# Optimization experiments

Measured on AMD Instinct MI355X. Metric: run time of the kernel, lower is better.

## Reference

```python
import jax, jax.numpy as jnp
import numpy as np


def _pairwise_sqdist(a, b):
    # a: [B,N,3], b: [B,M,3] -> [B,N,M] squared L2 distances
    a2 = jnp.sum(a * a, axis=-1)            # [B,N]
    b2 = jnp.sum(b * b, axis=-1)            # [B,M]
    ab = jnp.einsum('bnd,bmd->bnm', a, b)   # [B,N,M]
    d = a2[:, :, None] + b2[:, None, :] - 2.0 * ab
    return jnp.maximum(d, 0.0)


def setup_inputs() -> dict:
    key = jax.random.key(0)
    k1, k2 = jax.random.split(key)
    B, N, M = 4, 8192, 8192
    p1 = jax.random.normal(k1, (B, N, 3), dtype=jnp.float32)
    p2 = jax.random.normal(k2, (B, M, 3), dtype=jnp.float32)
    return {"p1": p1, "p2": p2}


def reference(p1, p2):
    # chamfer_3DDist: squared L2 NN distances both directions, then mean of each
    d = _pairwise_sqdist(p1, p2)   # [B,N,M]
    d1 = jnp.min(d, axis=2)        # [B,N] nearest p2 for each p1 point
    d2 = jnp.min(d, axis=1)        # [B,M] nearest p1 for each p2 point
    return jnp.mean(d1) + jnp.mean(d2)
```

## Files before the change

kernel.cpp:

```cpp
#include <hip/hip_runtime.h>
#include <float.h>


#define BLK 256
#define CHUNK 2048
#define QPT 2
#define QPB (BLK * QPT)
#define B 4
#define NPTS 8192
#define TOTQ (2 * B * NPTS)

__global__ __launch_bounds__(BLK) void init_kernel(unsigned* mins, float* out, int n) {
    int i = blockIdx.x * BLK + threadIdx.x;
    if (i < n) mins[i] = 0x7F7FFFFFu;
    if (i == 0) out[0] = 0.f;
}

__global__ __launch_bounds__(BLK) void zero_out_kernel(float* out) {
    if (threadIdx.x == 0 && blockIdx.x == 0) out[0] = 0.f;
}

__global__ __launch_bounds__(BLK, 2) void cd_chunk_kernel(
    const float* __restrict__ p1, const float* __restrict__ p2,
    unsigned* __restrict__ mins)
{
    __shared__ float4 pts[CHUNK];
    int bid    = blockIdx.x;
    int mchunk = bid & 3;
    int qt     = (bid >> 2) & 15;
    int batch  = (bid >> 6) & 3;
    int dir    = bid >> 8;

    const float* qbase = (dir == 0 ? p1 : p2) + (size_t)batch * NPTS * 3;
    const float* dbase = (dir == 0 ? p2 : p1) + (size_t)batch * NPTS * 3;

    int tid = threadIdx.x;
    int mstart = mchunk * CHUNK;
    for (int j = tid; j < CHUNK; j += BLK) {
        const float* s = dbase + (size_t)(mstart + j) * 3;
        float x = s[0], y = s[1], z = s[2];
        pts[j] = make_float4(x, y, z, -0.5f * (x * x + y * y + z * z));
    }

    int q0 = qt * QPB + tid;
    int q1 = q0 + BLK;
    float ax = qbase[q0 * 3 + 0], ay = qbase[q0 * 3 + 1], az = qbase[q0 * 3 + 2];
    float bx = qbase[q1 * 3 + 0], by = qbase[q1 * 3 + 1], bz = qbase[q1 * 3 + 2];
    float an = ax * ax + ay * ay + az * az;
    float bn = bx * bx + by * by + bz * bz;
    __syncthreads();

    float sa0 = -FLT_MAX, sa1 = -FLT_MAX;
    float sb0 = -FLT_MAX, sb1 = -FLT_MAX;
    #pragma unroll 4
    for (int j = 0; j < CHUNK; j += 2) {
        float4 u = pts[j];
        float4 v = pts[j + 1];
        float s;
        s = fmaf(ax, u.x, u.w); s = fmaf(ay, u.y, s); s = fmaf(az, u.z, s); sa0 = fmaxf(sa0, s);
        s = fmaf(bx, u.x, u.w); s = fmaf(by, u.y, s); s = fmaf(bz, u.z, s); sb0 = fmaxf(sb0, s);
        s = fmaf(ax, v.x, v.w); s = fmaf(ay, v.y, s); s = fmaf(az, v.z, s); sa1 = fmaxf(sa1, s);
        s = fmaf(bx, v.x, v.w); s = fmaf(by, v.y, s); s = fmaf(bz, v.z, s); sb1 = fmaxf(sb1, s);
    }
    float da = fmaxf(an - 2.f * fmaxf(sa0, sa1), 0.f);
    float db = fmaxf(bn - 2.f * fmaxf(sb0, sb1), 0.f);

    unsigned qid0 = (unsigned)(dir * (B * NPTS) + batch * NPTS + q0);
    atomicMin(&mins[qid0], __float_as_uint(da));
    atomicMin(&mins[qid0 + BLK], __float_as_uint(db));
}

__global__ __launch_bounds__(BLK) void sum_kernel(
    const unsigned* __restrict__ mins, float* __restrict__ out, int n, float scale)
{
    int i = blockIdx.x * BLK + threadIdx.x;
    int stride = gridDim.x * BLK;
    float v = 0.f;
    for (int idx = i; idx < n; idx += stride) v += __uint_as_float(mins[idx]);
    for (int off = 32; off > 0; off >>= 1) v += __shfl_down(v, off, 64);
    __shared__ float wsum[BLK / 64];
    int lane = threadIdx.x & 63, wid = threadIdx.x >> 6;
    if (lane == 0) wsum[wid] = v;
    __syncthreads();
    if (threadIdx.x == 0) {
        float t = 0.f;
        for (int w = 0; w < BLK / 64; ++w) t += wsum[w];
        atomicAdd(out, t * scale);
    }
}

__global__ __launch_bounds__(BLK) void cd_full_kernel(
    const float* __restrict__ p1, const float* __restrict__ p2,
    float* __restrict__ out)
{
    __shared__ float4 pts[CHUNK];
    int bid   = blockIdx.x;
    int qt    = bid & 15;
    int batch = (bid >> 4) & 3;
    int dir   = bid >> 6;

    const float* qbase = (dir == 0 ? p1 : p2) + (size_t)batch * NPTS * 3;
    const float* dbase = (dir == 0 ? p2 : p1) + (size_t)batch * NPTS * 3;

    int tid = threadIdx.x;
    int q0 = qt * QPB + tid;
    int q1 = q0 + BLK;
    float ax = qbase[q0 * 3 + 0], ay = qbase[q0 * 3 + 1], az = qbase[q0 * 3 + 2];
    float bx = qbase[q1 * 3 + 0], by = qbase[q1 * 3 + 1], bz = qbase[q1 * 3 + 2];
    float an = ax * ax + ay * ay + az * az;
    float bn = bx * bx + by * by + bz * bz;

    float sa = -FLT_MAX, sb = -FLT_MAX;
    for (int c = 0; c < 4; ++c) {
        __syncthreads();
        int mstart = c * CHUNK;
        for (int j = tid; j < CHUNK; j += BLK) {
            const float* s = dbase + (size_t)(mstart + j) * 3;
            float x = s[0], y = s[1], z = s[2];
            pts[j] = make_float4(x, y, z, -0.5f * (x * x + y * y + z * z));
        }
        __syncthreads();
        #pragma unroll 4
        for (int j = 0; j < CHUNK; j += 2) {
            float4 u = pts[j];
            float4 v = pts[j + 1];
            float s;
            s = fmaf(ax, u.x, u.w); s = fmaf(ay, u.y, s); s = fmaf(az, u.z, s); sa = fmaxf(sa, s);
            s = fmaf(bx, u.x, u.w); s = fmaf(by, u.y, s); s = fmaf(bz, u.z, s); sb = fmaxf(sb, s);
            s = fmaf(ax, v.x, v.w); s = fmaf(ay, v.y, s); s = fmaf(az, v.z, s); sa = fmaxf(sa, s);
            s = fmaf(bx, v.x, v.w); s = fmaf(by, v.y, s); s = fmaf(bz, v.z, s); sb = fmaxf(sb, s);
        }
    }
    float da = fmaxf(an - 2.f * sa, 0.f);
    float db = fmaxf(bn - 2.f * sb, 0.f);
    float v = da + db;
    for (int off = 32; off > 0; off >>= 1) v += __shfl_down(v, off, 64);
    __shared__ float wsum[BLK / 64];
    int lane = threadIdx.x & 63, wid = threadIdx.x >> 6;
    if (lane == 0) wsum[wid] = v;
    __syncthreads();
    if (threadIdx.x == 0) {
        float t = 0.f;
        for (int w = 0; w < BLK / 64; ++w) t += wsum[w];
        atomicAdd(out, t * (1.f / (float)(B * NPTS)));
    }
}

extern "C" void kernel_launch(void* const* d_in, const int* in_sizes, int n_in,
                              void* d_out, int out_size, void* d_ws, size_t ws_size,
                              hipStream_t stream) {
    const float* p1 = (const float*)d_in[0];
    const float* p2 = (const float*)d_in[1];
    float* out = (float*)d_out;

    if (ws_size >= (size_t)TOTQ * sizeof(unsigned)) {
        unsigned* mins = (unsigned*)d_ws;
        init_kernel<<<(TOTQ + BLK - 1) / BLK, BLK, 0, stream>>>(mins, out, TOTQ);
        cd_chunk_kernel<<<512, BLK, 0, stream>>>(p1, p2, mins);
        sum_kernel<<<64, BLK, 0, stream>>>(mins, out, TOTQ, 1.f / (float)(B * NPTS));
    } else {
        zero_out_kernel<<<1, BLK, 0, stream>>>(out);
        cd_full_kernel<<<128, BLK, 0, stream>>>(p1, p2, out);
    }
}
```

Before: 109.4 us.

## Split reference set into 8 chunks and vectorize chunk staging loads

```diff
diff --git a/kernel.cpp b/kernel.cpp
--- a/kernel.cpp
+++ b/kernel.cpp
@@ -2,44 +2,52 @@
 #include <float.h>
 
 
-#define BLK 256
-#define CHUNK 2048
-#define QPT 2
-#define QPB (BLK * QPT)
-#define B 4
-#define NPTS 8192
-#define TOTQ (2 * B * NPTS)
+#define BLK   256
+#define QPT   2
+#define QPB   (BLK * QPT)
+#define BATCH 4
+#define NPTS  8192
+#define NCH   8
+#define CHUNK (NPTS / NCH)
+#define QTILES (NPTS / QPB)
+#define GRID  (2 * BATCH * QTILES * NCH)
+#define TOTQ  (2 * BATCH * NPTS)
 
-__global__ __launch_bounds__(BLK) void init_kernel(unsigned* mins, float* out, int n) {
+__global__ __launch_bounds__(BLK) void init_kernel(unsigned* mins, int n) {
     int i = blockIdx.x * BLK + threadIdx.x;
     if (i < n) mins[i] = 0x7F7FFFFFu;
-    if (i == 0) out[0] = 0.f;
 }
 
-__global__ __launch_bounds__(BLK) void zero_out_kernel(float* out) {
-    if (threadIdx.x == 0 && blockIdx.x == 0) out[0] = 0.f;
-}
-
-__global__ __launch_bounds__(BLK, 2) void cd_chunk_kernel(
+__global__ __launch_bounds__(BLK, 4) void cd_chunk_kernel(
     const float* __restrict__ p1, const float* __restrict__ p2,
     unsigned* __restrict__ mins)
 {
     __shared__ float4 pts[CHUNK];
     int bid    = blockIdx.x;
-    int mchunk = bid & 3;
-    int qt     = (bid >> 2) & 15;
-    int batch  = (bid >> 6) & 3;
-    int dir    = bid >> 8;
+    int mchunk = bid & (NCH - 1);
+    int qt     = (bid >> 3) & (QTILES - 1);
+    int batch  = (bid >> 7) & (BATCH - 1);
+    int dir    = bid >> 9;
 
     const float* qbase = (dir == 0 ? p1 : p2) + (size_t)batch * NPTS * 3;
     const float* dbase = (dir == 0 ? p2 : p1) + (size_t)batch * NPTS * 3;
 
     int tid = threadIdx.x;
-    int mstart = mchunk * CHUNK;
-    for (int j = tid; j < CHUNK; j += BLK) {
-        const float* s = dbase + (size_t)(mstart + j) * 3;
-        float x = s[0], y = s[1], z = s[2];
-        pts[j] = make_float4(x, y, z, -0.5f * (x * x + y * y + z * z));
+
+    {
+        int t4 = tid * 4;
+        const float* s = dbase + (size_t)(mchunk * CHUNK + t4) * 3;
+        float4 f0 = *(const float4*)(s);
+        float4 f1 = *(const float4*)(s + 4);
+        float4 f2 = *(const float4*)(s + 8);
+        float x0 = f0.x, y0 = f0.y, z0 = f0.z;
+        float x1 = f0.w, y1 = f1.x, z1 = f1.y;
+        float x2 = f1.z, y2 = f1.w, z2 = f2.x;
+        float x3 = f2.y, y3 = f2.z, z3 = f2.w;
+        pts[t4 + 0] = make_float4(x0, y0, z0, -0.5f * (x0*x0 + y0*y0 + z0*z0));
+        pts[t4 + 1] = make_float4(x1, y1, z1, -0.5f * (x1*x1 + y1*y1 + z1*z1));
+        pts[t4 + 2] = make_float4(x2, y2, z2, -0.5f * (x2*x2 + y2*y2 + z2*z2));
+        pts[t4 + 3] = make_float4(x3, y3, z3, -0.5f * (x3*x3 + y3*y3 + z3*z3));
     }
 
     int q0 = qt * QPB + tid;
@@ -52,22 +60,35 @@
 
     float sa0 = -FLT_MAX, sa1 = -FLT_MAX;
     float sb0 = -FLT_MAX, sb1 = -FLT_MAX;
-    #pragma unroll 4
-    for (int j = 0; j < CHUNK; j += 2) {
-        float4 u = pts[j];
-        float4 v = pts[j + 1];
-        float s;
-        s = fmaf(ax, u.x, u.w); s = fmaf(ay, u.y, s); s = fmaf(az, u.z, s); sa0 = fmaxf(sa0, s);
-        s = fmaf(bx, u.x, u.w); s = fmaf(by, u.y, s); s = fmaf(bz, u.z, s); sb0 = fmaxf(sb0, s);
-        s = fmaf(ax, v.x, v.w); s = fmaf(ay, v.y, s); s = fmaf(az, v.z, s); sa1 = fmaxf(sa1, s);
-        s = fmaf(bx, v.x, v.w); s = fmaf(by, v.y, s); s = fmaf(bz, v.z, s); sb1 = fmaxf(sb1, s);
+
+    #pragma unroll 2
+    for (int j = 0; j < CHUNK; j += 4) {
+        float4 u0 = pts[j + 0];
+        float4 u1 = pts[j + 1];
+        float4 u2 = pts[j + 2];
+        float4 u3 = pts[j + 3];
+
+        float a0 = fmaf(az, u0.z, fmaf(ay, u0.y, fmaf(ax, u0.x, u0.w)));
+        float a1 = fmaf(az, u1.z, fmaf(ay, u1.y, fmaf(ax, u1.x, u1.w)));
+        float a2 = fmaf(az, u2.z, fmaf(ay, u2.y, fmaf(ax, u2.x, u2.w)));
+        float a3 = fmaf(az, u3.z, fmaf(ay, u3.y, fmaf(ax, u3.x, u3.w)));
+        sa0 = fmaxf(sa0, fmaxf(a0, a1));
+        sa1 = fmaxf(sa1, fmaxf(a2, a3));
+
+        float b0 = fmaf(bz, u0.z, fmaf(by, u0.y, fmaf(bx, u0.x, u0.w)));
+        float b1 = fmaf(bz, u1.z, fmaf(by, u1.y, fmaf(bx, u1.x, u1.w)));
+        float b2 = fmaf(bz, u2.z, fmaf(by, u2.y, fmaf(bx, u2.x, u2.w)));
+        float b3 = fmaf(bz, u3.z, fmaf(by, u3.y, fmaf(bx, u3.x, u3.w)));
+        sb0 = fmaxf(sb0, fmaxf(b0, b1));
+        sb1 = fmaxf(sb1, fmaxf(b2, b3));
     }
+
     float da = fmaxf(an - 2.f * fmaxf(sa0, sa1), 0.f);
     float db = fmaxf(bn - 2.f * fmaxf(sb0, sb1), 0.f);
 
-    unsigned qid0 = (unsigned)(dir * (B * NPTS) + batch * NPTS + q0);
-    atomicMin(&mins[qid0], __float_as_uint(da));
-    atomicMin(&mins[qid0 + BLK], __float_as_uint(db));
+    unsigned qid = (unsigned)(dir * (BATCH * NPTS) + batch * NPTS + q0);
+    atomicMin(&mins[qid], __float_as_uint(da));
+    atomicMin(&mins[qid + BLK], __float_as_uint(db));
 }
 
 __global__ __launch_bounds__(BLK) void sum_kernel(
@@ -89,11 +110,13 @@
     }
 }
 
+__global__ void zero_out_kernel(float* out) { out[0] = 0.f; }
+
 __global__ __launch_bounds__(BLK) void cd_full_kernel(
     const float* __restrict__ p1, const float* __restrict__ p2,
     float* __restrict__ out)
 {
-    __shared__ float4 pts[CHUNK];
+    __shared__ float4 pts[2048];
     int bid   = blockIdx.x;
     int qt    = bid & 15;
     int batch = (bid >> 4) & 3;
@@ -103,7 +126,7 @@
     const float* dbase = (dir == 0 ? p2 : p1) + (size_t)batch * NPTS * 3;
 
     int tid = threadIdx.x;
-    int q0 = qt * QPB + tid;
+    int q0 = qt * 512 + tid;
     int q1 = q0 + BLK;
     float ax = qbase[q0 * 3 + 0], ay = qbase[q0 * 3 + 1], az = qbase[q0 * 3 + 2];
     float bx = qbase[q1 * 3 + 0], by = qbase[q1 * 3 + 1], bz = qbase[q1 * 3 + 2];
@@ -113,15 +136,15 @@
     float sa = -FLT_MAX, sb = -FLT_MAX;
     for (int c = 0; c < 4; ++c) {
         __syncthreads();
-        int mstart = c * CHUNK;
-        for (int j = tid; j < CHUNK; j += BLK) {
+        int mstart = c * 2048;
+        for (int j = tid; j < 2048; j += BLK) {
             const float* s = dbase + (size_t)(mstart + j) * 3;
             float x = s[0], y = s[1], z = s[2];
             pts[j] = make_float4(x, y, z, -0.5f * (x * x + y * y + z * z));
         }
         __syncthreads();
         #pragma unroll 4
-        for (int j = 0; j < CHUNK; j += 2) {
+        for (int j = 0; j < 2048; j += 2) {
             float4 u = pts[j];
             float4 v = pts[j + 1];
             float s;
@@ -142,7 +165,7 @@
     if (threadIdx.x == 0) {
         float t = 0.f;
         for (int w = 0; w < BLK / 64; ++w) t += wsum[w];
-        atomicAdd(out, t * (1.f / (float)(B * NPTS)));
+        atomicAdd(out, t * (1.f / (float)(BATCH * NPTS)));
     }
 }
 
@@ -155,11 +178,12 @@
 
     if (ws_size >= (size_t)TOTQ * sizeof(unsigned)) {
         unsigned* mins = (unsigned*)d_ws;
-        init_kernel<<<(TOTQ + BLK - 1) / BLK, BLK, 0, stream>>>(mins, out, TOTQ);
-        cd_chunk_kernel<<<512, BLK, 0, stream>>>(p1, p2, mins);
-        sum_kernel<<<64, BLK, 0, stream>>>(mins, out, TOTQ, 1.f / (float)(B * NPTS));
+        init_kernel<<<TOTQ / BLK, BLK, 0, stream>>>(mins, TOTQ);
+        zero_out_kernel<<<1, 1, 0, stream>>>(out);
+        cd_chunk_kernel<<<GRID, BLK, 0, stream>>>(p1, p2, mins);
+        sum_kernel<<<64, BLK, 0, stream>>>(mins, out, TOTQ, 1.f / (float)(BATCH * NPTS));
     } else {
-        zero_out_kernel<<<1, BLK, 0, stream>>>(out);
+        zero_out_kernel<<<1, 1, 0, stream>>>(out);
         cd_full_kernel<<<128, BLK, 0, stream>>>(p1, p2, out);
     }
 }
```

New measurement: 107.0 us. 1.02x faster.
